# Optimization experiments

Hardware: AMD Instinct MI355X
Metric: run time of the kernel (lower is better)

The kernel has to match this reference:

```python
import jax, jax.numpy as jnp
import numpy as np

N_NODES = 50000
N_EDGES = 1600000
NIN = 64
NATT = 64
NHEAD = 4
D_K = NATT // NHEAD  # 16


def setup_inputs() -> dict:
    key = jax.random.key(0)
    ks = jax.random.split(key, 9)
    x = jax.random.normal(ks[0], (N_NODES, NIN), dtype=jnp.float32)
    edge = jax.random.randint(ks[1], (2, N_EDGES), 0, N_NODES, dtype=jnp.int32)
    s = 0.05
    Wq = jax.random.normal(ks[2], (NIN, NATT), dtype=jnp.float32) * s
    bq = jax.random.normal(ks[3], (NATT,), dtype=jnp.float32) * s
    Wk = jax.random.normal(ks[4], (NIN, NATT), dtype=jnp.float32) * s
    bk = jax.random.normal(ks[5], (NATT,), dtype=jnp.float32) * s
    Wv = jax.random.normal(ks[6], (NIN, NATT), dtype=jnp.float32) * s
    bv = jax.random.normal(ks[7], (NATT,), dtype=jnp.float32) * s
    return {"x": x, "edge": edge, "Wq": Wq, "bq": bq, "Wk": Wk, "bk": bk,
            "Wv": Wv, "bv": bv}


def _heads(h):
    # [N, natt] -> view(-1, nhead, d_k).transpose(1, 2) -> [N, d_k, nhead]
    n = h.shape[0]
    return h.reshape(n, NHEAD, D_K).transpose(0, 2, 1)


def reference(x, edge, Wq, bq, Wk, bk, Wv, bv):
    n = x.shape[0]
    q = _heads(x @ Wq + bq)  # [N, d_k, nhead]
    k = _heads(x @ Wk + bk)
    v = _heads(x @ Wv + bv)

    src = q[edge[0]]    # [E, d_k, nhead] gather by source node
    dst_k = k[edge[1]]  # [E, d_k, nhead] gather by destination node

    # scaled dot product over the d_k axis -> [E, nhead]
    prods = jnp.sum(src * dst_k, axis=1) / jnp.sqrt(jnp.float32(D_K))

    # segment softmax grouped by edge[attention_norm_idx] (= edge[0])
    seg = edge[0]
    seg_max = jax.ops.segment_max(prods, seg, num_segments=n)      # [N, nhead]
    ex = jnp.exp(prods - seg_max[seg])                              # [E, nhead]
    denom = jax.ops.segment_sum(ex, seg, num_segments=n)           # [N, nhead]
    attention = ex / (denom[seg] + jnp.float32(1e-16))

    return attention, v, prods
```

## Files before the change

### kernel.cpp

```cpp
#include <hip/hip_runtime.h>
#include <hip/hip_bf16.h>

#define NHEAD 4

typedef __hip_bfloat16 bf16;
typedef __hip_bfloat162 bf162;

__global__ __launch_bounds__(256) void qkv_kernel(
    const float* __restrict__ x,
    const float* __restrict__ Wq, const float* __restrict__ bq,
    const float* __restrict__ Wk, const float* __restrict__ bk,
    const float* __restrict__ Wv, const float* __restrict__ bv,
    bf16* __restrict__ qout, bf16* __restrict__ kout,
    float* __restrict__ vout, int n_nodes) {
  __shared__ float xs[16][64];
  const int t = threadIdx.x;
  const int base = blockIdx.x * 16;
#pragma unroll
  for (int j = 0; j < 4; ++j) {
    const int idx = t + 256 * j;
    const int nn = idx >> 6, cc = idx & 63;
    xs[nn][cc] = (base + nn < n_nodes) ? x[(size_t)(base + nn) * 64 + cc] : 0.f;
  }
  __syncthreads();
  const int c = t & 63;
  const int qg = t >> 6;

  float aq[4], ak[4], av[4];
  const float bqv = bq[c], bkv = bk[c], bvv = bv[c];
#pragma unroll
  for (int j = 0; j < 4; ++j) { aq[j] = bqv; ak[j] = bkv; av[j] = bvv; }

#pragma unroll 4
  for (int r = 0; r < 64; ++r) {
    const float wq = Wq[r * 64 + c];
    const float wk = Wk[r * 64 + c];
    const float wv = Wv[r * 64 + c];
#pragma unroll
    for (int j = 0; j < 4; ++j) {
      const float xv = xs[qg * 4 + j][r];
      aq[j] = fmaf(xv, wq, aq[j]);
      ak[j] = fmaf(xv, wk, ak[j]);
      av[j] = fmaf(xv, wv, av[j]);
    }
  }
#pragma unroll
  for (int j = 0; j < 4; ++j) {
    const int node = base + qg * 4 + j;
    if (node < n_nodes) {
      qout[(size_t)node * 64 + c] = __float2bfloat16(aq[j]);
      kout[(size_t)node * 64 + c] = __float2bfloat16(ak[j]);
      vout[(size_t)node * 64 + (c & 15) * 4 + (c >> 4)] = av[j];
    }
  }
}

__device__ __forceinline__ float dot8(uint4 a, uint4 b) {
  const unsigned* pa = &a.x;
  const unsigned* pb = &b.x;
  float acc = 0.f;
#pragma unroll
  for (int i = 0; i < 4; ++i) {
    const float2 fa = __bfloat1622float2(*(const bf162*)&pa[i]);
    const float2 fb = __bfloat1622float2(*(const bf162*)&pb[i]);
    acc = fmaf(fa.x, fb.x, acc);
    acc = fmaf(fa.y, fb.y, acc);
  }
  return acc;
}

__global__ __launch_bounds__(256) void edge_kernel(
    const int* __restrict__ edge0, const int* __restrict__ edge1,
    const uint4* __restrict__ q, const uint4* __restrict__ k,
    float* __restrict__ prods, float* __restrict__ denom, int n_edges) {
  const long long i = (long long)blockIdx.x * 256 + threadIdx.x;
  const int e = (int)(i >> 2);
  const int h = (int)(i & 3);
  if (e >= n_edges) return;
  const int src = edge0[e];
  const int dst = edge1[e];

  const uint4 a0 = q[(size_t)src * 8 + h * 2];
  const uint4 a1 = q[(size_t)src * 8 + h * 2 + 1];
  const uint4 b0 = k[(size_t)dst * 8 + h * 2];
  const uint4 b1 = k[(size_t)dst * 8 + h * 2 + 1];

  const float p = (dot8(a0, b0) + dot8(a1, b1)) * 0.25f;
  prods[i] = p;
  atomicAdd(&denom[src * 4 + h], __expf(p));
}

__global__ __launch_bounds__(256) void norm_kernel(
    const int* __restrict__ edge0, const float* __restrict__ denom,
    const float* __restrict__ prods, float* __restrict__ attn, long long n4) {
  const long long i = (long long)blockIdx.x * 256 + threadIdx.x;
  if (i >= n4) return;
  const int e = (int)(i >> 2);
  const int h = (int)(i & 3);
  const int seg = edge0[e];
  attn[i] = __expf(prods[i]) / (denom[seg * 4 + h] + 1e-16f);
}

extern "C" void kernel_launch(void* const* d_in, const int* in_sizes, int n_in,
                              void* d_out, int out_size, void* d_ws, size_t ws_size,
                              hipStream_t stream) {
  const float* x  = (const float*)d_in[0];
  const int* edge = (const int*)d_in[1];
  const float* Wq = (const float*)d_in[2];
  const float* bq = (const float*)d_in[3];
  const float* Wk = (const float*)d_in[4];
  const float* bk = (const float*)d_in[5];
  const float* Wv = (const float*)d_in[6];
  const float* bv = (const float*)d_in[7];

  const int n_nodes = in_sizes[0] / 64;
  const int n_edges = in_sizes[1] / 2;
  const int* edge0 = edge;
  const int* edge1 = edge + n_edges;

  float* out_attn  = (float*)d_out;
  float* out_v     = out_attn + (long long)n_edges * NHEAD;
  float* out_prods = out_v + (long long)n_nodes * 64;

  bf16* ws_q = (bf16*)d_ws;
  bf16* ws_k = ws_q + (size_t)n_nodes * 64;
  float* ws_denom = (float*)(ws_k + (size_t)n_nodes * 64);

  hipMemsetAsync(ws_denom, 0, (size_t)n_nodes * NHEAD * sizeof(float), stream);

  {
    const int blocks = (n_nodes + 15) / 16;
    qkv_kernel<<<blocks, 256, 0, stream>>>(x, Wq, bq, Wk, bk, Wv, bv,
                                           ws_q, ws_k, out_v, n_nodes);
  }
  {
    const long long total = (long long)n_edges * NHEAD;
    const int blocks = (int)((total + 255) / 256);
    edge_kernel<<<blocks, 256, 0, stream>>>(edge0, edge1,
                                            (const uint4*)ws_q, (const uint4*)ws_k,
                                            out_prods, ws_denom, n_edges);
    norm_kernel<<<blocks, 256, 0, stream>>>(edge0, ws_denom, out_prods,
                                            out_attn, total);
  }
}
```

Measured before the change: 218.7 us.

## Use head-major Q/K/denom layout and per-head edge passes with nontemporal I/O

Stores Q, K and the softmax denominators in head-major layout and runs the edge kernel one head per block range, so each head's gather hits a smaller working set (about 1.6 MB per head) that fits in cache better. Products go to a head-major workspace and the norm kernel transposes them back, writing attention and prods as float4 vectors. The denominator memset is folded into the QKV kernel, and nontemporal loads and stores are added for streaming data. The cost is an extra workspace round trip for prods and reading the edge indices four times. The in-kernel zeroing relies on the QKV grid having enough threads, which holds here because blocks×256 is well above n_nodes×4.

```diff
diff --git a/kernel.cpp b/kernel.cpp
--- a/kernel.cpp
+++ b/kernel.cpp
@@ -5,6 +5,7 @@
 
 typedef __hip_bfloat16 bf16;
 typedef __hip_bfloat162 bf162;
+typedef float f32x4 __attribute__((ext_vector_type(4)));
 
 __global__ __launch_bounds__(256) void qkv_kernel(
     const float* __restrict__ x,
@@ -12,7 +13,10 @@
     const float* __restrict__ Wk, const float* __restrict__ bk,
     const float* __restrict__ Wv, const float* __restrict__ bv,
     bf16* __restrict__ qout, bf16* __restrict__ kout,
-    float* __restrict__ vout, int n_nodes) {
+    float* __restrict__ vout, float* __restrict__ denom, int n_nodes) {
+  const long long gtid = (long long)blockIdx.x * 256 + threadIdx.x;
+  if (gtid < (long long)n_nodes * NHEAD) denom[gtid] = 0.f;
+
   __shared__ float xs[16][64];
   const int t = threadIdx.x;
   const int base = blockIdx.x * 16;
@@ -20,7 +24,9 @@
   for (int j = 0; j < 4; ++j) {
     const int idx = t + 256 * j;
     const int nn = idx >> 6, cc = idx & 63;
-    xs[nn][cc] = (base + nn < n_nodes) ? x[(size_t)(base + nn) * 64 + cc] : 0.f;
+    xs[nn][cc] = (base + nn < n_nodes)
+                     ? __builtin_nontemporal_load(&x[(size_t)(base + nn) * 64 + cc])
+                     : 0.f;
   }
   __syncthreads();
   const int c = t & 63;
@@ -44,13 +50,14 @@
       av[j] = fmaf(xv, wv, av[j]);
     }
   }
+  const int h = c >> 4, d = c & 15;
 #pragma unroll
   for (int j = 0; j < 4; ++j) {
     const int node = base + qg * 4 + j;
     if (node < n_nodes) {
-      qout[(size_t)node * 64 + c] = __float2bfloat16(aq[j]);
-      kout[(size_t)node * 64 + c] = __float2bfloat16(ak[j]);
-      vout[(size_t)node * 64 + (c & 15) * 4 + (c >> 4)] = av[j];
+      qout[((size_t)h * n_nodes + node) * 16 + d] = __float2bfloat16(aq[j]);
+      kout[((size_t)h * n_nodes + node) * 16 + d] = __float2bfloat16(ak[j]);
+      __builtin_nontemporal_store(av[j], &vout[(size_t)node * 64 + d * 4 + h]);
     }
   }
 }
@@ -72,33 +79,41 @@
 __global__ __launch_bounds__(256) void edge_kernel(
     const int* __restrict__ edge0, const int* __restrict__ edge1,
     const uint4* __restrict__ q, const uint4* __restrict__ k,
-    float* __restrict__ prods, float* __restrict__ denom, int n_edges) {
-  const long long i = (long long)blockIdx.x * 256 + threadIdx.x;
-  const int e = (int)(i >> 2);
-  const int h = (int)(i & 3);
+    float* __restrict__ prods_t, float* __restrict__ denom,
+    int n_edges, int n_nodes, int bph) {
+  const int h = blockIdx.x / bph;
+  const int e = (blockIdx.x - h * bph) * 256 + threadIdx.x;
   if (e >= n_edges) return;
-  const int src = edge0[e];
-  const int dst = edge1[e];
+  const int src = __builtin_nontemporal_load(&edge0[e]);
+  const int dst = __builtin_nontemporal_load(&edge1[e]);
 
-  const uint4 a0 = q[(size_t)src * 8 + h * 2];
-  const uint4 a1 = q[(size_t)src * 8 + h * 2 + 1];
-  const uint4 b0 = k[(size_t)dst * 8 + h * 2];
-  const uint4 b1 = k[(size_t)dst * 8 + h * 2 + 1];
+  const size_t qb = ((size_t)h * n_nodes + src) * 2;
+  const size_t kb = ((size_t)h * n_nodes + dst) * 2;
+  const uint4 a0 = q[qb], a1 = q[qb + 1];
+  const uint4 b0 = k[kb], b1 = k[kb + 1];
 
   const float p = (dot8(a0, b0) + dot8(a1, b1)) * 0.25f;
-  prods[i] = p;
-  atomicAdd(&denom[src * 4 + h], __expf(p));
+  __builtin_nontemporal_store(p, &prods_t[(size_t)h * n_edges + e]);
+  atomicAdd(&denom[h * n_nodes + src], __expf(p));
 }
 
 __global__ __launch_bounds__(256) void norm_kernel(
     const int* __restrict__ edge0, const float* __restrict__ denom,
-    const float* __restrict__ prods, float* __restrict__ attn, long long n4) {
-  const long long i = (long long)blockIdx.x * 256 + threadIdx.x;
-  if (i >= n4) return;
-  const int e = (int)(i >> 2);
-  const int h = (int)(i & 3);
-  const int seg = edge0[e];
-  attn[i] = __expf(prods[i]) / (denom[seg * 4 + h] + 1e-16f);
+    const float* __restrict__ prods_t, f32x4* __restrict__ attn4,
+    f32x4* __restrict__ prods4, int n_edges, int n_nodes) {
+  const int e = blockIdx.x * 256 + threadIdx.x;
+  if (e >= n_edges) return;
+  const int seg = __builtin_nontemporal_load(&edge0[e]);
+  float p[4], a[4];
+#pragma unroll
+  for (int h = 0; h < 4; ++h) {
+    p[h] = __builtin_nontemporal_load(&prods_t[(size_t)h * n_edges + e]);
+    a[h] = __expf(p[h]) / (denom[h * n_nodes + seg] + 1e-16f);
+  }
+  const f32x4 av = {a[0], a[1], a[2], a[3]};
+  const f32x4 pv = {p[0], p[1], p[2], p[3]};
+  __builtin_nontemporal_store(av, &attn4[e]);
+  __builtin_nontemporal_store(pv, &prods4[e]);
 }
 
 extern "C" void kernel_launch(void* const* d_in, const int* in_sizes, int n_in,
@@ -123,23 +138,25 @@
   float* out_prods = out_v + (long long)n_nodes * 64;
 
   bf16* ws_q = (bf16*)d_ws;
-  bf16* ws_k = ws_q + (size_t)n_nodes * 64;
-  float* ws_denom = (float*)(ws_k + (size_t)n_nodes * 64);
-
-  hipMemsetAsync(ws_denom, 0, (size_t)n_nodes * NHEAD * sizeof(float), stream);
+  bf16* ws_k = ws_q + (size_t)NHEAD * n_nodes * 16;
+  float* ws_prods = (float*)(ws_k + (size_t)NHEAD * n_nodes * 16);
+  float* ws_denom = ws_prods + (size_t)NHEAD * n_edges;
 
   {
     const int blocks = (n_nodes + 15) / 16;
     qkv_kernel<<<blocks, 256, 0, stream>>>(x, Wq, bq, Wk, bk, Wv, bv,
-                                           ws_q, ws_k, out_v, n_nodes);
+                                           ws_q, ws_k, out_v, ws_denom, n_nodes);
   }
   {
-    const long long total = (long long)n_edges * NHEAD;
-    const int blocks = (int)((total + 255) / 256);
-    edge_kernel<<<blocks, 256, 0, stream>>>(edge0, edge1,
-                                            (const uint4*)ws_q, (const uint4*)ws_k,
-                                            out_prods, ws_denom, n_edges);
-    norm_kernel<<<blocks, 256, 0, stream>>>(edge0, ws_denom, out_prods,
-                                            out_attn, total);
+    const int bph = (n_edges + 255) / 256;
+    edge_kernel<<<bph * NHEAD, 256, 0, stream>>>(
+        edge0, edge1, (const uint4*)ws_q, (const uint4*)ws_k,
+        ws_prods, ws_denom, n_edges, n_nodes, bph);
+  }
+  {
+    const int blocks = (n_edges + 255) / 256;
+    norm_kernel<<<blocks, 256, 0, stream>>>(edge0, ws_denom, ws_prods,
+                                            (f32x4*)out_attn, (f32x4*)out_prods,
+                                            n_edges, n_nodes);
   }
 }
```

After: 504.2 us. 131% more time.

## Fuse edge and norm kernels with a grid barrier; zero denom in qkv kernel

Applied to the files above, without the earlier changes.

Merges the edge-score and normalization kernels into one persistent grid-stride kernel of 2048 blocks that synchronizes through a global atomic counter barrier, so the second launch goes away. The denom zeroing memset becomes part of the qkv kernel, leaving only a 4-byte counter memset, and x is read with nontemporal loads. The software grid barrier assumes all 2048 blocks are resident at once (launch bounds allow 8 per CU), otherwise it deadlocks. The persistent loop also gives up some of the parallelism of the one-thread-per-pair launch.

```diff
diff --git a/kernel.cpp b/kernel.cpp
--- a/kernel.cpp
+++ b/kernel.cpp
@@ -2,9 +2,12 @@
 #include <hip/hip_bf16.h>
 
 #define NHEAD 4
+#define NT 256
+#define NB 2048
 
 typedef __hip_bfloat16 bf16;
 typedef __hip_bfloat162 bf162;
+typedef float f32x4 __attribute__((ext_vector_type(4)));
 
 __global__ __launch_bounds__(256) void qkv_kernel(
     const float* __restrict__ x,
@@ -12,7 +15,10 @@
     const float* __restrict__ Wk, const float* __restrict__ bk,
     const float* __restrict__ Wv, const float* __restrict__ bv,
     bf16* __restrict__ qout, bf16* __restrict__ kout,
-    float* __restrict__ vout, int n_nodes) {
+    float* __restrict__ vout, float* __restrict__ denom, int n_nodes) {
+  const long long gtid = (long long)blockIdx.x * 256 + threadIdx.x;
+  if (gtid < (long long)n_nodes * NHEAD) denom[gtid] = 0.f;
+
   __shared__ float xs[16][64];
   const int t = threadIdx.x;
   const int base = blockIdx.x * 16;
@@ -20,7 +26,9 @@
   for (int j = 0; j < 4; ++j) {
     const int idx = t + 256 * j;
     const int nn = idx >> 6, cc = idx & 63;
-    xs[nn][cc] = (base + nn < n_nodes) ? x[(size_t)(base + nn) * 64 + cc] : 0.f;
+    xs[nn][cc] = (base + nn < n_nodes)
+                     ? __builtin_nontemporal_load(&x[(size_t)(base + nn) * 64 + cc])
+                     : 0.f;
   }
   __syncthreads();
   const int c = t & 63;
@@ -69,36 +77,48 @@
   return acc;
 }
 
-__global__ __launch_bounds__(256) void edge_kernel(
+__global__ __launch_bounds__(NT, 8) void edge_norm_kernel(
     const int* __restrict__ edge0, const int* __restrict__ edge1,
-    const uint4* __restrict__ q, const uint4* __restrict__ k,
-    float* __restrict__ prods, float* __restrict__ denom, int n_edges) {
-  const long long i = (long long)blockIdx.x * 256 + threadIdx.x;
-  const int e = (int)(i >> 2);
-  const int h = (int)(i & 3);
-  if (e >= n_edges) return;
-  const int src = edge0[e];
-  const int dst = edge1[e];
+    const uint4* __restrict__ q4, const uint4* __restrict__ k4,
+    float* __restrict__ prods, float* __restrict__ attn,
+    float* __restrict__ denom, unsigned* __restrict__ counter, int n_edges) {
+  const int gid = blockIdx.x * NT + threadIdx.x;
+  const int nthreads = NB * NT;
+  const long long npairs = (long long)n_edges * NHEAD;
 
-  const uint4 a0 = q[(size_t)src * 8 + h * 2];
-  const uint4 a1 = q[(size_t)src * 8 + h * 2 + 1];
-  const uint4 b0 = k[(size_t)dst * 8 + h * 2];
-  const uint4 b1 = k[(size_t)dst * 8 + h * 2 + 1];
+  for (long long i = gid; i < npairs; i += nthreads) {
+    const int e = (int)(i >> 2);
+    const int h = (int)(i & 3);
+    const int src = edge0[e];
+    const int dst = edge1[e];
+    const size_t qb = (size_t)src * 8 + h * 2;
+    const size_t kb = (size_t)dst * 8 + h * 2;
+    const uint4 a0 = q4[qb], a1 = q4[qb + 1];
+    const uint4 b0 = k4[kb], b1 = k4[kb + 1];
+    const float p = (dot8(a0, b0) + dot8(a1, b1)) * 0.25f;
+    prods[i] = p;
+    atomicAdd(&denom[(size_t)src * 4 + h], __expf(p));
+  }
 
-  const float p = (dot8(a0, b0) + dot8(a1, b1)) * 0.25f;
-  prods[i] = p;
-  atomicAdd(&denom[src * 4 + h], __expf(p));
-}
+  __syncthreads();
+  if (threadIdx.x == 0) {
+    __hip_atomic_fetch_add(counter, 1u, __ATOMIC_RELEASE,
+                           __HIP_MEMORY_SCOPE_AGENT);
+    while (__hip_atomic_load(counter, __ATOMIC_RELAXED,
+                             __HIP_MEMORY_SCOPE_AGENT) < NB)
+      __builtin_amdgcn_s_sleep(16);
+    __threadfence();
+  }
+  __syncthreads();
 
-__global__ __launch_bounds__(256) void norm_kernel(
-    const int* __restrict__ edge0, const float* __restrict__ denom,
-    const float* __restrict__ prods, float* __restrict__ attn, long long n4) {
-  const long long i = (long long)blockIdx.x * 256 + threadIdx.x;
-  if (i >= n4) return;
-  const int e = (int)(i >> 2);
-  const int h = (int)(i & 3);
-  const int seg = edge0[e];
-  attn[i] = __expf(prods[i]) / (denom[seg * 4 + h] + 1e-16f);
+  for (long long i = gid; i < npairs; i += nthreads) {
+    const int e = (int)(i >> 2);
+    const int h = (int)(i & 3);
+    const int seg = edge0[e];
+    const float p = prods[i];
+    const float den = denom[(size_t)seg * 4 + h];
+    attn[i] = __expf(p) / (den + 1e-16f);
+  }
 }
 
 extern "C" void kernel_launch(void* const* d_in, const int* in_sizes, int n_in,
@@ -125,21 +145,18 @@
   bf16* ws_q = (bf16*)d_ws;
   bf16* ws_k = ws_q + (size_t)n_nodes * 64;
   float* ws_denom = (float*)(ws_k + (size_t)n_nodes * 64);
+  unsigned* ws_counter = (unsigned*)(ws_denom + (size_t)n_nodes * NHEAD);
 
-  hipMemsetAsync(ws_denom, 0, (size_t)n_nodes * NHEAD * sizeof(float), stream);
+  hipMemsetAsync(ws_counter, 0, sizeof(unsigned), stream);
 
   {
     const int blocks = (n_nodes + 15) / 16;
     qkv_kernel<<<blocks, 256, 0, stream>>>(x, Wq, bq, Wk, bk, Wv, bv,
-                                           ws_q, ws_k, out_v, n_nodes);
+                                           ws_q, ws_k, out_v, ws_denom, n_nodes);
   }
   {
-    const long long total = (long long)n_edges * NHEAD;
-    const int blocks = (int)((total + 255) / 256);
-    edge_kernel<<<blocks, 256, 0, stream>>>(edge0, edge1,
-                                            (const uint4*)ws_q, (const uint4*)ws_k,
-                                            out_prods, ws_denom, n_edges);
-    norm_kernel<<<blocks, 256, 0, stream>>>(edge0, ws_denom, out_prods,
-                                            out_attn, total);
+    edge_norm_kernel<<<NB, NT, 0, stream>>>(
+        edge0, edge1, (const uint4*)ws_q, (const uint4*)ws_k,
+        out_prods, out_attn, ws_denom, ws_counter, n_edges);
   }
 }
```

Result: slower. 503.2 us (+130.0%).
